# Kernel optimization log

Hardware: AMD Instinct MI355X
Metric: run time of the kernel (lower is better)

The kernel has to match this reference:

```python
import jax, jax.numpy as jnp
import numpy as np

KS = 3          # kernel_size
PAD = KS // 2   # =1, symmetric pad (pd=2, pdr=1 in the original)


def setup_inputs() -> dict:
    key = jax.random.key(0)
    k1, k2 = jax.random.split(key)
    B, H, W, T, C = 1, 48, 48, 48, 32
    q = jax.random.normal(k1, (B, H, W, T, C), dtype=jnp.float32)
    k = jax.random.normal(k2, (B, H, W, T, C), dtype=jnp.float32)
    return {"q": q, "k": k}


def reference(q, k):
    # q, k: [B, H, W, T, C]
    B, H, W, T, C = q.shape
    # zero-pad k spatially by 1 on each side (matches nnf.pad with pdr=1)
    kp = jnp.pad(k, ((0, 0), (PAD, PAD), (PAD, PAD), (PAD, PAD), (0, 0)))
    # gather the 27 shifted windows; token order (dh major, dt minor) matches
    # unfold(1).unfold(2).unfold(3) + permute in the original.
    wins = jnp.stack(
        [kp[:, a:a + H, b:b + W, c:c + T, :]
         for a in range(KS) for b in range(KS) for c in range(KS)],
        axis=4,
    )  # [B, H, W, T, 27, C]
    # QK^T over channel dim -> [B, H, W, T, 27]
    scores = jnp.einsum('bhwtc,bhwtjc->bhwtj', q, wins)
    attn = jax.nn.softmax(scores, axis=-1)
    # fixed displacement grid v: offsets (-1,0,1)^3 in (dh, dw, dt) order
    ax = jnp.arange(-(KS // 2), KS // 2 + 1, dtype=q.dtype)  # [-1, 0, 1]
    offs = jnp.stack(jnp.meshgrid(ax, ax, ax, indexing='ij'), axis=-1)
    offs = offs.reshape(KS ** 3, 3)  # [27, 3]
    # displacement-weighted sum -> [B, H, W, T, 3]
    x = jnp.einsum('bhwtj,jd->bhwtd', attn, offs)
    # -> [B, 3, H, W, T]
    return jnp.transpose(x, (0, 4, 1, 2, 3))
```

## Files before the change

kernel.cpp:

```cpp
#include <hip/hip_runtime.h>
#include <hip/hip_bf16.h>
#include <math.h>

#define DH 48
#define DW 48
#define DT 48
#define DC 32
#define NPOS (DH * DW * DT)

__global__ __launch_bounds__(192) void cotr_natt_kernel(
    const float* __restrict__ q,
    const float* __restrict__ k,
    float* __restrict__ out)
{
    const int h = blockIdx.x / DW;
    const int w = blockIdx.x - h * DW;
    const int t = threadIdx.x >> 2;
    const int sub = threadIdx.x & 3;

    const int idx = (h * DW + w) * DT + t;

    const float4* qp = reinterpret_cast<const float4*>(q + (size_t)idx * DC);
    const float4 q0 = qp[sub * 2];
    const float4 q1 = qp[sub * 2 + 1];

    float part[27];
#pragma unroll
    for (int a = 0; a < 3; ++a) {
        const int hh = h + a - 1;
        const bool va = ((unsigned)hh < DH);
#pragma unroll
        for (int b = 0; b < 3; ++b) {
            const int ww = w + b - 1;
            const bool vb = va && ((unsigned)ww < DW);
            const int rowbase = (hh * DW + ww) * DT;
#pragma unroll
            for (int c = 0; c < 3; ++c) {
                const int tt = t + c - 1;
                const int j = (a * 3 + b) * 3 + c;
                float s = 0.0f;
                if (vb && ((unsigned)tt < DT)) {
                    const float4* kp = reinterpret_cast<const float4*>(
                        k + (size_t)(rowbase + tt) * DC);
                    const float4 k0 = kp[sub * 2];
                    const float4 k1 = kp[sub * 2 + 1];
                    s = fmaf(q0.x, k0.x,
                        fmaf(q0.y, k0.y,
                        fmaf(q0.z, k0.z,
                        fmaf(q0.w, k0.w,
                        fmaf(q1.x, k1.x,
                        fmaf(q1.y, k1.y,
                        fmaf(q1.z, k1.z, q1.w * k1.w)))))));
                }
                part[j] = s;
            }
        }
    }

    float m = -INFINITY;
#pragma unroll
    for (int j = 0; j < 27; ++j) {
        float v = part[j];
        v += __shfl_xor(v, 1, 64);
        v += __shfl_xor(v, 2, 64);
        part[j] = v;
        m = fmaxf(m, v);
    }

    float sum = 0.0f;
    float oh = 0.0f, ow = 0.0f, ot = 0.0f;
#pragma unroll
    for (int j = 0; j < 27; ++j) {
        const float e = __expf(part[j] - m);
        sum += e;
        const float da = (float)(j / 9 - 1);
        const float db = (float)((j / 3) % 3 - 1);
        const float dc = (float)(j % 3 - 1);
        oh = fmaf(e, da, oh);
        ow = fmaf(e, db, ow);
        ot = fmaf(e, dc, ot);
    }
    const float inv = 1.0f / sum;

    if (sub == 0)       out[0 * NPOS + idx] = oh * inv;
    else if (sub == 1)  out[1 * NPOS + idx] = ow * inv;
    else if (sub == 2)  out[2 * NPOS + idx] = ot * inv;
}

extern "C" void kernel_launch(void* const* d_in, const int* in_sizes, int n_in,
                              void* d_out, int out_size, void* d_ws, size_t ws_size,
                              hipStream_t stream) {
    const float* q = reinterpret_cast<const float*>(d_in[0]);
    const float* k = reinterpret_cast<const float*>(d_in[1]);
    float* out = reinterpret_cast<float*>(d_out);

    const int threads = 192;
    const int blocks = DH * DW;
    cotr_natt_kernel<<<blocks, threads, 0, stream>>>(q, k, out);
}
```

Measured before the change: 90.12 us.

## Stage 3x3 neighbor k rows in LDS with zero-padded time halo

Each block now cooperatively loads the nine neighboring (h,w) rows of k into shared memory, padding one zero slot at each end of the time axis so the inner loop needs no bounds checks. Each k element is then read from global memory once per block instead of three times across the time offsets. Blocks grow to 384 threads with 8 lanes per position, so each lane holds one float4 of q and the reduction gains one more shuffle step. This costs about 57 KB of LDS per block and a barrier, which limits how many blocks can be resident per CU.

```diff
diff --git a/kernel.cpp b/kernel.cpp
--- a/kernel.cpp
+++ b/kernel.cpp
@@ -7,53 +7,60 @@
 #define DT 48
 #define DC 32
 #define NPOS (DH * DW * DT)
+#define TSLOTS 50
 
-__global__ __launch_bounds__(192) void cotr_natt_kernel(
+__global__ __launch_bounds__(384) void cotr_natt_kernel(
     const float* __restrict__ q,
     const float* __restrict__ k,
     float* __restrict__ out)
 {
+    __shared__ float kl[9 * TSLOTS * DC];
+
     const int h = blockIdx.x / DW;
     const int w = blockIdx.x - h * DW;
-    const int t = threadIdx.x >> 2;
-    const int sub = threadIdx.x & 3;
+    const int tid = threadIdx.x;
 
+    const int st = tid >> 3;
+    const int sc = tid & 7;
+#pragma unroll
+    for (int r = 0; r < 9; ++r) {
+        const int hh = h + r / 3 - 1;
+        const int ww = w + r % 3 - 1;
+        float4 v = make_float4(0.f, 0.f, 0.f, 0.f);
+        if (((unsigned)hh < DH) & ((unsigned)ww < DW)) {
+            v = *reinterpret_cast<const float4*>(
+                k + ((size_t)(hh * DW + ww) * DT + st) * DC + sc * 4);
+        }
+        *reinterpret_cast<float4*>(&kl[(r * TSLOTS + 1 + st) * DC + sc * 4]) = v;
+    }
+    if (tid < 144) {
+        const int r = tid >> 4;
+        const int rem = tid & 15;
+        const int slot = (rem >> 3) ? (TSLOTS - 1) : 0;
+        const int c4 = rem & 7;
+        *reinterpret_cast<float4*>(&kl[(r * TSLOTS + slot) * DC + c4 * 4]) =
+            make_float4(0.f, 0.f, 0.f, 0.f);
+    }
+    __syncthreads();
+
+    const int t = tid >> 3;
+    const int sub = tid & 7;
     const int idx = (h * DW + w) * DT + t;
 
-    const float4* qp = reinterpret_cast<const float4*>(q + (size_t)idx * DC);
-    const float4 q0 = qp[sub * 2];
-    const float4 q1 = qp[sub * 2 + 1];
+    const float4 qv =
+        *reinterpret_cast<const float4*>(q + (size_t)idx * DC + sub * 4);
 
     float part[27];
 #pragma unroll
-    for (int a = 0; a < 3; ++a) {
-        const int hh = h + a - 1;
-        const bool va = ((unsigned)hh < DH);
+    for (int r = 0; r < 9; ++r) {
 #pragma unroll
-        for (int b = 0; b < 3; ++b) {
-            const int ww = w + b - 1;
-            const bool vb = va && ((unsigned)ww < DW);
-            const int rowbase = (hh * DW + ww) * DT;
-#pragma unroll
-            for (int c = 0; c < 3; ++c) {
-                const int tt = t + c - 1;
-                const int j = (a * 3 + b) * 3 + c;
-                float s = 0.0f;
-                if (vb && ((unsigned)tt < DT)) {
-                    const float4* kp = reinterpret_cast<const float4*>(
-                        k + (size_t)(rowbase + tt) * DC);
-                    const float4 k0 = kp[sub * 2];
-                    const float4 k1 = kp[sub * 2 + 1];
-                    s = fmaf(q0.x, k0.x,
-                        fmaf(q0.y, k0.y,
-                        fmaf(q0.z, k0.z,
-                        fmaf(q0.w, k0.w,
-                        fmaf(q1.x, k1.x,
-                        fmaf(q1.y, k1.y,
-                        fmaf(q1.z, k1.z, q1.w * k1.w)))))));
-                }
-                part[j] = s;
-            }
+        for (int c = 0; c < 3; ++c) {
+            const float4 kv = *reinterpret_cast<const float4*>(
+                &kl[(r * TSLOTS + t + c) * DC + sub * 4]);
+            part[r * 3 + c] =
+                fmaf(qv.x, kv.x,
+                fmaf(qv.y, kv.y,
+                fmaf(qv.z, kv.z, qv.w * kv.w)));
         }
     }
 
@@ -63,6 +70,7 @@
         float v = part[j];
         v += __shfl_xor(v, 1, 64);
         v += __shfl_xor(v, 2, 64);
+        v += __shfl_xor(v, 4, 64);
         part[j] = v;
         m = fmaxf(m, v);
     }
@@ -82,9 +90,9 @@
     }
     const float inv = 1.0f / sum;
 
-    if (sub == 0)       out[0 * NPOS + idx] = oh * inv;
-    else if (sub == 1)  out[1 * NPOS + idx] = ow * inv;
-    else if (sub == 2)  out[2 * NPOS + idx] = ot * inv;
+    if (sub == 0)      out[0 * NPOS + idx] = oh * inv;
+    else if (sub == 1) out[1 * NPOS + idx] = ow * inv;
+    else if (sub == 2) out[2 * NPOS + idx] = ot * inv;
 }
 
 extern "C" void kernel_launch(void* const* d_in, const int* in_sizes, int n_in,
@@ -94,7 +102,7 @@
     const float* k = reinterpret_cast<const float*>(d_in[1]);
     float* out = reinterpret_cast<float*>(d_out);
 
-    const int threads = 192;
+    const int threads = 384;
     const int blocks = DH * DW;
     cotr_natt_kernel<<<blocks, threads, 0, stream>>>(q, k, out);
 }
```

Result: slower. 109.8 us (+21.9%).
